# Kernel optimization log

Measured on AMD Instinct MI355X. Metric: run time of the kernel, lower is better.

The kernel has to match this reference:

```python
import jax, jax.numpy as jnp
import numpy as np

NX, NY = 384, 384
H = 1e-4
DT = 5e-9
NT = 192
STRIDE = 4
RHO = 1610.0
F0 = 2.0e6
T0 = 4e-7
AMP = 1e10
GAUSS_A = 5e6

C11_INIT, C22_INIT, C12_INIT = 1.3074e11, 1.15e10, 1.049e10
C16_INIT, C26_INIT, C66_INIT = 3.067e10, 3.75e9, 1.477e10
B11 = (5e10, 2.5e11); B22 = (5e9, 5e10); B12 = (5e9, 5e10)
B16 = (0.0, 6e10); B26 = (0.0, 2e10); B66 = (5e9, 3e10)


def setup_inputs() -> dict:
    # log-parameter fields, constant-initialized as in the module __init__
    full = lambda v: jnp.full((1, NX, NY), np.log(v), dtype=jnp.float32)
    log_C11 = full(C11_INIT)
    log_C22 = full(C22_INIT)
    log_C12 = full(C12_INIT)
    log_C16 = full(abs(C16_INIT) + 1e6)
    log_C26 = full(abs(C26_INIT) + 1e6)
    log_C66 = full(C66_INIT)
    # Gaussian point-load distribution centered at domain center
    Lx, Ly = H * (NX - 1), H * (NY - 1)
    x = np.linspace(-Lx / 2, Lx / 2, NX)
    y = np.linspace(-Ly / 2, Ly / 2, NY)
    X, Y = np.meshgrid(x, y, indexing='ij')
    gauss = (GAUSS_A / np.pi) * np.exp(-GAUSS_A * (X ** 2 + Y ** 2))
    # Ricker wavelet source signal over nt steps
    t = np.arange(NT) * DT
    tau = t - T0
    pft2 = (np.pi * F0 * tau) ** 2
    sig = AMP * (1.0 - 2.0 * pft2) * np.exp(-pft2)
    return {
        'log_C11': log_C11, 'log_C12': log_C12, 'log_C16': log_C16,
        'log_C22': log_C22, 'log_C26': log_C26, 'log_C66': log_C66,
        'gaussian_dist': jnp.asarray(gauss, dtype=jnp.float32),
        'source_signal': jnp.asarray(sig, dtype=jnp.float32),
    }


def _stencils(u, hinv2):
    # u: (B, nx, ny). Zero padding == fixed (u=0) boundary, matching conv2d_fixed.
    up = jnp.pad(u, ((0, 0), (1, 1), (1, 1)))
    d2x = (up[:, :-2, 1:-1] - 2.0 * u + up[:, 2:, 1:-1]) * hinv2
    d2y = (up[:, 1:-1, :-2] - 2.0 * u + up[:, 1:-1, 2:]) * hinv2
    dxy = 0.25 * (up[:, :-2, :-2] - up[:, :-2, 2:] - up[:, 2:, :-2] + up[:, 2:, 2:]) * hinv2
    return d2x, d2y, dxy


def _simulate(log_C11, log_C12, log_C16, log_C22, log_C26, log_C66,
              gaussian_dist, source_signal):
    clip = lambda lc, b: jnp.clip(jnp.exp(lc), b[0], b[1])
    C11 = clip(log_C11, B11); C22 = clip(log_C22, B22); C12 = clip(log_C12, B12)
    C16 = clip(log_C16, B16); C26 = clip(log_C26, B26); C66 = clip(log_C66, B66)
    hinv2 = jnp.float32(1.0 / (H * H))
    dt2 = jnp.float32(DT * DT)
    g = gaussian_dist[None]  # (1, nx, ny)
    C12p66 = C12 + C66

    def step(carry, sig_t):
        ux1, uy1, ux2, uy2 = carry
        dxx_x, dyy_x, dxy_x = _stencils(ux1, hinv2)
        dxx_y, dyy_y, dxy_y = _stencils(uy1, hinv2)
        Lux = (C11 * dxx_x + C66 * dyy_x + C12p66 * dxy_y
               + 2.0 * C16 * dxy_x + C16 * dxx_y + C26 * dyy_y)
        Luy = (C66 * dxx_y + C22 * dyy_y + C12p66 * dxy_x
               + C16 * dxx_x + C26 * dyy_x + 2.0 * C26 * dxy_y)
        # Ricker point source on the y-component (source_component='y')
        ax = Lux / RHO
        ay = (Luy + sig_t * g) / RHO
        ux_new = 2.0 * ux1 - ux2 + dt2 * ax
        uy_new = 2.0 * uy1 - uy2 + dt2 * ay
        return (ux_new, uy_new, ux1, uy1), (ux_new, uy_new)

    z = jnp.zeros((1, NX, NY), dtype=jnp.float32)
    _, (ux_all, uy_all) = jax.lax.scan(step, (z, z, z, z), source_signal)
    # subsample by primary_time_stride -> (1, nt//stride, nx, ny)
    ux_f = jnp.transpose(ux_all[STRIDE - 1::STRIDE], (1, 0, 2, 3))
    uy_f = jnp.transpose(uy_all[STRIDE - 1::STRIDE], (1, 0, 2, 3))
    return jnp.stack([ux_f, uy_f])  # (2, 1, nt_out, nx, ny)


def reference(log_C11, log_C12, log_C16, log_C22, log_C26, log_C66,
              gaussian_dist, source_signal):
    return _simulate(log_C11, log_C12, log_C16, log_C22, log_C26, log_C66,
                     gaussian_dist, source_signal)
```

## Files before the change

kernel.cpp:

```cpp
#include <hip/hip_runtime.h>


typedef float v2f __attribute__((ext_vector_type(2)));

#define NXg 384
#define NYg 384
#define NPT (NXg * NYg)
#define NFRAMES 48

#define OWN 24
#define HALO 12
#define TS 48
#define KSTEPS 12
#define NLAUNCH 16

#define H_   1e-4
#define DT_  5e-9
#define RHO_ 1610.0

#define B11_LO 5e10f
#define B11_HI 2.5e11f
#define B22_LO 5e9f
#define B22_HI 5e10f
#define B12_LO 5e9f
#define B12_HI 5e10f
#define B16_LO 0.0f
#define B16_HI 6e10f
#define B26_LO 0.0f
#define B26_HI 2e10f
#define B66_LO 5e9f
#define B66_HI 3e10f

static __device__ __constant__ float kScale  = (float)(DT_ * DT_ / (H_ * H_) / RHO_);
static __device__ __constant__ float kSrcScl = (float)(DT_ * DT_ / RHO_);

__device__ __forceinline__ float clipf(float v, float lo, float hi) {
    return fminf(fmaxf(v, lo), hi);
}
__device__ __forceinline__ v2f vfma(v2f a, v2f b, v2f c) {
    return __builtin_elementwise_fma(a, b, c);
}
__device__ __forceinline__ v2f vbc(float s) { v2f r; r[0] = s; r[1] = s; return r; }
__device__ __forceinline__ v2f vswap(v2f a) { return __builtin_shufflevector(a, a, 1, 0); }

#define LDS_BARRIER() asm volatile("s_waitcnt lgkmcnt(0)\n\ts_barrier" ::: "memory")


__global__ __launch_bounds__(256)
void setup_kernel(const float* __restrict__ lc11, const float* __restrict__ lc12,
                  const float* __restrict__ lc16, const float* __restrict__ lc22,
                  const float* __restrict__ lc26, const float* __restrict__ lc66,
                  const float* __restrict__ gauss, float* __restrict__ ws) {
    int i = blockIdx.x * blockDim.x + threadIdx.x;
    if (i >= NPT) return;
    float C11 = clipf(expf(lc11[i]), B11_LO, B11_HI);
    float C12 = clipf(expf(lc12[i]), B12_LO, B12_HI);
    float C16 = clipf(expf(lc16[i]), B16_LO, B16_HI);
    float C22 = clipf(expf(lc22[i]), B22_LO, B22_HI);
    float C26 = clipf(expf(lc26[i]), B26_LO, B26_HI);
    float C66 = clipf(expf(lc66[i]), B66_LO, B66_HI);
    float s = kScale;
    float4* C0 = (float4*)ws;
    float4* C1 = (float4*)(ws + 4 * (size_t)NPT);
    C0[i] = make_float4(C11 * s, C22 * s, (C12 + C66) * s, C16 * s);
    C1[i] = make_float4(C26 * s, C66 * s, gauss[i] * kSrcScl, 0.0f);
    float4* s0 = (float4*)(ws + 8 * (size_t)NPT);
    s0[i] = make_float4(0.0f, 0.0f, 0.0f, 0.0f);
}

__global__ __launch_bounds__(256, 1)
void fused_kernel(const float* __restrict__ ws, const float* __restrict__ sig,
                  const float4* __restrict__ inS, float4* __restrict__ outS,
                  float* __restrict__ out, int L) {
    __shared__ v2f sb[2][TS][TS + 1];

    const int tid = threadIdx.x;
    const int tx = tid >> 4;
    const int ty = tid & 15;
    const int r0 = 3 * tx;
    const int c0 = 3 * ty;
    const int gx0 = blockIdx.y * OWN - HALO;
    const int gy0 = blockIdx.x * OWN - HALO;

    const float4* __restrict__ C0 = (const float4*)ws;
    const float4* __restrict__ C1 = (const float4*)(ws + 4 * (size_t)NPT);

    v2f cur[9], old_[9];
    v2f ca[9], cb[9];
    float a12p66[9], a16[9], a26[9], gs[9];
    int gidx[9];

#pragma unroll
    for (int i = 0; i < 3; ++i) {
#pragma unroll
        for (int j = 0; j < 3; ++j) {
            int p = i * 3 + j;
            int gx = gx0 + r0 + i;
            int gy = gy0 + c0 + j;
            bool d = (unsigned)gx < (unsigned)NXg && (unsigned)gy < (unsigned)NYg;
            int g = d ? gx * NYg + gy : 0;
            gidx[p] = g;
            float4 st = d ? inS[g] : make_float4(0, 0, 0, 0);
            v2f c; c[0] = st.x; c[1] = st.y;
            v2f o; o[0] = st.z; o[1] = st.w;
            cur[p] = c; old_[p] = o;
            float4 k0 = d ? C0[g] : make_float4(0, 0, 0, 0);
            float4 k1 = d ? C1[g] : make_float4(0, 0, 0, 0);
            v2f t; t[0] = k0.x; t[1] = k1.y; ca[p] = t;
            v2f u; u[0] = k1.y; u[1] = k0.y; cb[p] = u;
            a12p66[p] = k0.z; a16[p] = k0.w; a26[p] = k1.x; gs[p] = k1.z;
        }
    }

    const int t0 = L * KSTEPS;
    float sigv[KSTEPS];
#pragma unroll
    for (int k = 0; k < KSTEPS; ++k) sigv[k] = sig[t0 + k];

    const int rm = (r0 > 0) ? r0 - 1 : 0;
    const int rp = (r0 + 3 < TS) ? r0 + 3 : TS - 1;
    const int cm = (c0 > 0) ? c0 - 1 : 0;
    const int cp = (c0 + 3 < TS) ? c0 + 3 : TS - 1;

    const bool owned = (tx >= 4) && (tx < 12) && (ty >= 4) && (ty < 12);

#pragma unroll
    for (int i = 0; i < 3; ++i)
#pragma unroll
        for (int j = 0; j < 3; ++j)
            sb[0][r0 + i][c0 + j] = cur[i * 3 + j];
    LDS_BARRIER();

    v2f c20; c20[0] = 2.0f; c20[1] = 0.0f;
    v2f c02; c02[0] = 0.0f; c02[1] = 2.0f;
    const v2f m2 = vbc(-2.0f);
    const v2f qt = vbc(0.25f);
    const v2f two = vbc(2.0f);

#pragma unroll 1
    for (int s = 1; s <= KSTEPS; ++s) {
        const v2f (*rb)[TS + 1] = sb[(s - 1) & 1];
        v2f (*wb)[TS + 1] = sb[s & 1];
        v2f vsig; vsig[0] = 0.0f; vsig[1] = sigv[s - 1];

        v2f v[5][5];
#pragma unroll
        for (int i = 0; i < 3; ++i)
#pragma unroll
            for (int j = 0; j < 3; ++j)
                v[i + 1][j + 1] = cur[i * 3 + j];
        v[0][0] = rb[rm][cm];  v[0][4] = rb[rm][cp];
        v[4][0] = rb[rp][cm];  v[4][4] = rb[rp][cp];
#pragma unroll
        for (int j = 0; j < 3; ++j) {
            v[0][j + 1] = rb[rm][c0 + j];
            v[4][j + 1] = rb[rp][c0 + j];
            v[j + 1][0] = rb[r0 + j][cm];
            v[j + 1][4] = rb[r0 + j][cp];
        }

        v2f dh[5][3];
#pragma unroll
        for (int i = 0; i < 5; ++i)
#pragma unroll
            for (int j = 0; j < 3; ++j)
                dh[i][j] = v[i][j + 2] - v[i][j];

#pragma unroll
        for (int i = 0; i < 3; ++i)
#pragma unroll
            for (int j = 0; j < 3; ++j) {
                int p = i * 3 + j;
                v2f c = v[i + 1][j + 1];
                v2f sxx = vfma(m2, c, v[i][j + 1] + v[i + 2][j + 1]);
                v2f syy = vfma(m2, c, v[i + 1][j] + v[i + 1][j + 2]);
                v2f sxy = qt * (dh[i + 2][j] - dh[i][j]);

                v2f t4 = vfma(c20, vbc(sxy[0]), vswap(sxx));
                v2f t5 = vfma(c02, vbc(sxy[1]), vswap(syy));
                v2f Lv = ca[p] * sxx;
                Lv = vfma(cb[p], syy, Lv);
                Lv = vfma(vbc(a12p66[p]), vswap(sxy), Lv);
                Lv = vfma(vbc(a16[p]), t4, Lv);
                Lv = vfma(vbc(a26[p]), t5, Lv);
                Lv = vfma(vsig, vbc(gs[p]), Lv);
                v2f n = vfma(two, c, Lv) - old_[p];
                old_[p] = c;
                cur[p] = n;
            }

        if ((s & 3) == 0 && owned) {
            int f = 3 * L + (s >> 2) - 1;
            float* oux = out + (size_t)f * NPT;
            float* ouy = out + (size_t)(NFRAMES + f) * NPT;
#pragma unroll
            for (int p = 0; p < 9; ++p) {
                oux[gidx[p]] = cur[p][0];
                ouy[gidx[p]] = cur[p][1];
            }
        }

#pragma unroll
        for (int i = 0; i < 3; ++i)
#pragma unroll
            for (int j = 0; j < 3; ++j)
                wb[r0 + i][c0 + j] = cur[i * 3 + j];
        LDS_BARRIER();
    }

    if (owned) {
#pragma unroll
        for (int p = 0; p < 9; ++p) {
            float4 st = make_float4(cur[p][0], cur[p][1], old_[p][0], old_[p][1]);
            outS[gidx[p]] = st;
        }
    }
}

extern "C" void kernel_launch(void* const* d_in, const int* in_sizes, int n_in,
                              void* d_out, int out_size, void* d_ws, size_t ws_size,
                              hipStream_t stream) {
    const float* lc11  = (const float*)d_in[0];
    const float* lc12  = (const float*)d_in[1];
    const float* lc16  = (const float*)d_in[2];
    const float* lc22  = (const float*)d_in[3];
    const float* lc26  = (const float*)d_in[4];
    const float* lc66  = (const float*)d_in[5];
    const float* gauss = (const float*)d_in[6];
    const float* sig   = (const float*)d_in[7];

    float* ws  = (float*)d_ws;
    float* out = (float*)d_out;

    setup_kernel<<<(NPT + 255) / 256, 256, 0, stream>>>(lc11, lc12, lc16, lc22,
                                                        lc26, lc66, gauss, ws);

    float4* set0 = (float4*)(ws + 8 * (size_t)NPT);
    float4* set1 = (float4*)(ws + 12 * (size_t)NPT);

    dim3 grid(NXg / OWN, NYg / OWN);
    for (int L = 0; L < NLAUNCH; ++L) {
        float4* iS = (L & 1) ? set1 : set0;
        float4* oS = (L & 1) ? set0 : set1;
        fused_kernel<<<grid, 256, 0, stream>>>(ws, sig, iS, oS, out, L);
    }
}
```

Measured before the change: 354.5 us.

## Replace per-phase kernel launches with persistent kernel and grid barriers

Turns the 16 back-to-back fused_kernel launches into one persistent kernel that loops over all phases. Blocks exchange halo state through global double buffers and synchronise with an atomic-counter grid barrier. Only non-owned halo cells are reloaded after each barrier, and coefficients stay in registers across phases. This removes the launch gaps and the repeated coefficient and state reloads. In exchange it relies on all 256 blocks being co-resident and adds spin-wait barrier cost.

```diff
diff --git a/kernel.cpp b/kernel.cpp
--- a/kernel.cpp
+++ b/kernel.cpp
@@ -12,7 +12,8 @@
 #define HALO 12
 #define TS 48
 #define KSTEPS 12
-#define NLAUNCH 16
+#define NPHASE 16
+#define NBLK 256
 
 #define H_   1e-4
 #define DT_  5e-9
@@ -45,13 +46,28 @@
 
 #define LDS_BARRIER() asm volatile("s_waitcnt lgkmcnt(0)\n\ts_barrier" ::: "memory")
 
+__device__ __forceinline__ void grid_barrier(unsigned* cnt) {
+    __syncthreads();
+    if (threadIdx.x == 0) {
+        __threadfence();
+        __hip_atomic_fetch_add(cnt, 1u, __ATOMIC_ACQ_REL, __HIP_MEMORY_SCOPE_AGENT);
+        while (__hip_atomic_load(cnt, __ATOMIC_RELAXED, __HIP_MEMORY_SCOPE_AGENT) < NBLK) {
+            __builtin_amdgcn_s_sleep(2);
+        }
+        __threadfence();
+    }
+    __syncthreads();
+}
+
 
 __global__ __launch_bounds__(256)
 void setup_kernel(const float* __restrict__ lc11, const float* __restrict__ lc12,
                   const float* __restrict__ lc16, const float* __restrict__ lc22,
                   const float* __restrict__ lc26, const float* __restrict__ lc66,
-                  const float* __restrict__ gauss, float* __restrict__ ws) {
+                  const float* __restrict__ gauss, float* __restrict__ ws,
+                  unsigned* __restrict__ bar) {
     int i = blockIdx.x * blockDim.x + threadIdx.x;
+    if (i < 16) bar[i] = 0u;
     if (i >= NPT) return;
     float C11 = clipf(expf(lc11[i]), B11_LO, B11_HI);
     float C12 = clipf(expf(lc12[i]), B12_LO, B12_HI);
@@ -64,14 +80,13 @@
     float4* C1 = (float4*)(ws + 4 * (size_t)NPT);
     C0[i] = make_float4(C11 * s, C22 * s, (C12 + C66) * s, C16 * s);
     C1[i] = make_float4(C26 * s, C66 * s, gauss[i] * kSrcScl, 0.0f);
-    float4* s0 = (float4*)(ws + 8 * (size_t)NPT);
-    s0[i] = make_float4(0.0f, 0.0f, 0.0f, 0.0f);
 }
 
 __global__ __launch_bounds__(256, 1)
-void fused_kernel(const float* __restrict__ ws, const float* __restrict__ sig,
-                  const float4* __restrict__ inS, float4* __restrict__ outS,
-                  float* __restrict__ out, int L) {
+void fused_persistent(const float4* __restrict__ C0, const float4* __restrict__ C1,
+                      const float* __restrict__ sig,
+                      float4* xset0, float4* xset1, unsigned* bar,
+                      float* __restrict__ out) {
     __shared__ v2f sb[2][TS][TS + 1];
 
     const int tid = threadIdx.x;
@@ -82,13 +97,11 @@
     const int gx0 = blockIdx.y * OWN - HALO;
     const int gy0 = blockIdx.x * OWN - HALO;
 
-    const float4* __restrict__ C0 = (const float4*)ws;
-    const float4* __restrict__ C1 = (const float4*)(ws + 4 * (size_t)NPT);
-
     v2f cur[9], old_[9];
     v2f ca[9], cb[9];
     float a12p66[9], a16[9], a26[9], gs[9];
     int gidx[9];
+    int dmask = 0;
 
 #pragma unroll
     for (int i = 0; i < 3; ++i) {
@@ -100,10 +113,8 @@
             bool d = (unsigned)gx < (unsigned)NXg && (unsigned)gy < (unsigned)NYg;
             int g = d ? gx * NYg + gy : 0;
             gidx[p] = g;
-            float4 st = d ? inS[g] : make_float4(0, 0, 0, 0);
-            v2f c; c[0] = st.x; c[1] = st.y;
-            v2f o; o[0] = st.z; o[1] = st.w;
-            cur[p] = c; old_[p] = o;
+            if (d) dmask |= (1 << p);
+            cur[p] = vbc(0.0f); old_[p] = vbc(0.0f);
             float4 k0 = d ? C0[g] : make_float4(0, 0, 0, 0);
             float4 k1 = d ? C1[g] : make_float4(0, 0, 0, 0);
             v2f t; t[0] = k0.x; t[1] = k1.y; ca[p] = t;
@@ -112,24 +123,12 @@
         }
     }
 
-    const int t0 = L * KSTEPS;
-    float sigv[KSTEPS];
-#pragma unroll
-    for (int k = 0; k < KSTEPS; ++k) sigv[k] = sig[t0 + k];
-
     const int rm = (r0 > 0) ? r0 - 1 : 0;
     const int rp = (r0 + 3 < TS) ? r0 + 3 : TS - 1;
     const int cm = (c0 > 0) ? c0 - 1 : 0;
     const int cp = (c0 + 3 < TS) ? c0 + 3 : TS - 1;
 
     const bool owned = (tx >= 4) && (tx < 12) && (ty >= 4) && (ty < 12);
-
-#pragma unroll
-    for (int i = 0; i < 3; ++i)
-#pragma unroll
-        for (int j = 0; j < 3; ++j)
-            sb[0][r0 + i][c0 + j] = cur[i * 3 + j];
-    LDS_BARRIER();
 
     v2f c20; c20[0] = 2.0f; c20[1] = 0.0f;
     v2f c02; c02[0] = 0.0f; c02[1] = 2.0f;
@@ -138,81 +137,112 @@
     const v2f two = vbc(2.0f);
 
 #pragma unroll 1
-    for (int s = 1; s <= KSTEPS; ++s) {
-        const v2f (*rb)[TS + 1] = sb[(s - 1) & 1];
-        v2f (*wb)[TS + 1] = sb[s & 1];
-        v2f vsig; vsig[0] = 0.0f; vsig[1] = sigv[s - 1];
-
-        v2f v[5][5];
+    for (int L = 0; L < NPHASE; ++L) {
+        const int t0 = L * KSTEPS;
+        float sigv[KSTEPS];
+#pragma unroll
+        for (int k = 0; k < KSTEPS; ++k) sigv[k] = sig[t0 + k];
+
 #pragma unroll
         for (int i = 0; i < 3; ++i)
 #pragma unroll
             for (int j = 0; j < 3; ++j)
-                v[i + 1][j + 1] = cur[i * 3 + j];
-        v[0][0] = rb[rm][cm];  v[0][4] = rb[rm][cp];
-        v[4][0] = rb[rp][cm];  v[4][4] = rb[rp][cp];
-#pragma unroll
-        for (int j = 0; j < 3; ++j) {
-            v[0][j + 1] = rb[rm][c0 + j];
-            v[4][j + 1] = rb[rp][c0 + j];
-            v[j + 1][0] = rb[r0 + j][cm];
-            v[j + 1][4] = rb[r0 + j][cp];
-        }
-
-        v2f dh[5][3];
-#pragma unroll
-        for (int i = 0; i < 5; ++i)
-#pragma unroll
-            for (int j = 0; j < 3; ++j)
-                dh[i][j] = v[i][j + 2] - v[i][j];
-
-#pragma unroll
-        for (int i = 0; i < 3; ++i)
+                sb[0][r0 + i][c0 + j] = cur[i * 3 + j];
+        LDS_BARRIER();
+
+#pragma unroll 1
+        for (int s = 1; s <= KSTEPS; ++s) {
+            const v2f (*rb)[TS + 1] = sb[(s - 1) & 1];
+            v2f (*wb)[TS + 1] = sb[s & 1];
+            v2f vsig; vsig[0] = 0.0f; vsig[1] = sigv[s - 1];
+
+            v2f v[5][5];
+#pragma unroll
+            for (int i = 0; i < 3; ++i)
+#pragma unroll
+                for (int j = 0; j < 3; ++j)
+                    v[i + 1][j + 1] = cur[i * 3 + j];
+            v[0][0] = rb[rm][cm];  v[0][4] = rb[rm][cp];
+            v[4][0] = rb[rp][cm];  v[4][4] = rb[rp][cp];
 #pragma unroll
             for (int j = 0; j < 3; ++j) {
-                int p = i * 3 + j;
-                v2f c = v[i + 1][j + 1];
-                v2f sxx = vfma(m2, c, v[i][j + 1] + v[i + 2][j + 1]);
-                v2f syy = vfma(m2, c, v[i + 1][j] + v[i + 1][j + 2]);
-                v2f sxy = qt * (dh[i + 2][j] - dh[i][j]);
-
-                v2f t4 = vfma(c20, vbc(sxy[0]), vswap(sxx));
-                v2f t5 = vfma(c02, vbc(sxy[1]), vswap(syy));
-                v2f Lv = ca[p] * sxx;
-                Lv = vfma(cb[p], syy, Lv);
-                Lv = vfma(vbc(a12p66[p]), vswap(sxy), Lv);
-                Lv = vfma(vbc(a16[p]), t4, Lv);
-                Lv = vfma(vbc(a26[p]), t5, Lv);
-                Lv = vfma(vsig, vbc(gs[p]), Lv);
-                v2f n = vfma(two, c, Lv) - old_[p];
-                old_[p] = c;
-                cur[p] = n;
-            }
-
-        if ((s & 3) == 0 && owned) {
-            int f = 3 * L + (s >> 2) - 1;
-            float* oux = out + (size_t)f * NPT;
-            float* ouy = out + (size_t)(NFRAMES + f) * NPT;
-#pragma unroll
-            for (int p = 0; p < 9; ++p) {
-                oux[gidx[p]] = cur[p][0];
-                ouy[gidx[p]] = cur[p][1];
-            }
-        }
-
-#pragma unroll
-        for (int i = 0; i < 3; ++i)
-#pragma unroll
-            for (int j = 0; j < 3; ++j)
-                wb[r0 + i][c0 + j] = cur[i * 3 + j];
-        LDS_BARRIER();
-    }
-
-    if (owned) {
-#pragma unroll
-        for (int p = 0; p < 9; ++p) {
-            float4 st = make_float4(cur[p][0], cur[p][1], old_[p][0], old_[p][1]);
-            outS[gidx[p]] = st;
+                v[0][j + 1] = rb[rm][c0 + j];
+                v[4][j + 1] = rb[rp][c0 + j];
+                v[j + 1][0] = rb[r0 + j][cm];
+                v[j + 1][4] = rb[r0 + j][cp];
+            }
+
+            v2f dh[5][3];
+#pragma unroll
+            for (int i = 0; i < 5; ++i)
+#pragma unroll
+                for (int j = 0; j < 3; ++j)
+                    dh[i][j] = v[i][j + 2] - v[i][j];
+
+#pragma unroll
+            for (int i = 0; i < 3; ++i)
+#pragma unroll
+                for (int j = 0; j < 3; ++j) {
+                    int p = i * 3 + j;
+                    v2f c = v[i + 1][j + 1];
+                    v2f sxx = vfma(m2, c, v[i][j + 1] + v[i + 2][j + 1]);
+                    v2f syy = vfma(m2, c, v[i + 1][j] + v[i + 1][j + 2]);
+                    v2f sxy = qt * (dh[i + 2][j] - dh[i][j]);
+
+                    v2f t4 = vfma(c20, vbc(sxy[0]), vswap(sxx));
+                    v2f t5 = vfma(c02, vbc(sxy[1]), vswap(syy));
+                    v2f Lv = ca[p] * sxx;
+                    Lv = vfma(cb[p], syy, Lv);
+                    Lv = vfma(vbc(a12p66[p]), vswap(sxy), Lv);
+                    Lv = vfma(vbc(a16[p]), t4, Lv);
+                    Lv = vfma(vbc(a26[p]), t5, Lv);
+                    Lv = vfma(vsig, vbc(gs[p]), Lv);
+                    v2f n = vfma(two, c, Lv) - old_[p];
+                    old_[p] = c;
+                    cur[p] = n;
+                }
+
+            if ((s & 3) == 0 && owned) {
+                int f = 3 * L + (s >> 2) - 1;
+                float* oux = out + (size_t)f * NPT;
+                float* ouy = out + (size_t)(NFRAMES + f) * NPT;
+#pragma unroll
+                for (int p = 0; p < 9; ++p) {
+                    oux[gidx[p]] = cur[p][0];
+                    ouy[gidx[p]] = cur[p][1];
+                }
+            }
+
+#pragma unroll
+            for (int i = 0; i < 3; ++i)
+#pragma unroll
+                for (int j = 0; j < 3; ++j)
+                    wb[r0 + i][c0 + j] = cur[i * 3 + j];
+            LDS_BARRIER();
+        }
+
+        if (L + 1 < NPHASE) {
+            float4* xb = (L & 1) ? xset1 : xset0;
+            if (owned) {
+#pragma unroll
+                for (int p = 0; p < 9; ++p)
+                    xb[gidx[p]] = make_float4(cur[p][0], cur[p][1],
+                                              old_[p][0], old_[p][1]);
+            }
+            grid_barrier(bar + L);
+            if (!owned) {
+#pragma unroll
+                for (int p = 0; p < 9; ++p) {
+                    if ((dmask >> p) & 1) {
+                        float4 st = xb[gidx[p]];
+                        v2f c; c[0] = st.x; c[1] = st.y;
+                        v2f o; o[0] = st.z; o[1] = st.w;
+                        cur[p] = c; old_[p] = o;
+                    } else {
+                        cur[p] = vbc(0.0f); old_[p] = vbc(0.0f);
+                    }
+                }
+            }
         }
     }
 }
@@ -227,21 +257,20 @@
     const float* lc26  = (const float*)d_in[4];
     const float* lc66  = (const float*)d_in[5];
     const float* gauss = (const float*)d_in[6];
-    const float* sig   = (const float*)d_in[7];
+    const float* sigp  = (const float*)d_in[7];
 
     float* ws  = (float*)d_ws;
     float* out = (float*)d_out;
 
+    const float4* C0    = (const float4*)ws;
+    const float4* C1    = (const float4*)(ws + 4 * (size_t)NPT);
+    float4*       xset0 = (float4*)(ws + 8 * (size_t)NPT);
+    float4*       xset1 = (float4*)(ws + 12 * (size_t)NPT);
+    unsigned*     bar   = (unsigned*)(ws + 16 * (size_t)NPT);
+
     setup_kernel<<<(NPT + 255) / 256, 256, 0, stream>>>(lc11, lc12, lc16, lc22,
-                                                        lc26, lc66, gauss, ws);
-
-    float4* set0 = (float4*)(ws + 8 * (size_t)NPT);
-    float4* set1 = (float4*)(ws + 12 * (size_t)NPT);
+                                                        lc26, lc66, gauss, ws, bar);
 
     dim3 grid(NXg / OWN, NYg / OWN);
-    for (int L = 0; L < NLAUNCH; ++L) {
-        float4* iS = (L & 1) ? set1 : set0;
-        float4* oS = (L & 1) ? set0 : set1;
-        fused_kernel<<<grid, 256, 0, stream>>>(ws, sig, iS, oS, out, L);
-    }
-}
+    fused_persistent<<<grid, 256, 0, stream>>>(C0, C1, sigp, xset0, xset1, bar, out);
+}
```

Result: slower. 812.3 us (+129.1%).
